# Kernel tuning notes

Hardware: AMD Instinct MI355X
Metric: run time of the kernel (lower is better)

The kernel has to match this reference:

```python
import jax, jax.numpy as jnp
import numpy as np

B = 262144
H = 64  # hidden size
T = 64  # timesteps


def _linear_params(key, out_dim, in_dim):
    k1, k2 = jax.random.split(key)
    bound = 1.0 / np.sqrt(in_dim)
    w = jax.random.uniform(k1, (out_dim, in_dim), jnp.float32, -bound, bound)
    b = jax.random.uniform(k2, (out_dim,), jnp.float32, -bound, bound)
    return w, b


def setup_inputs() -> dict:
    key = jax.random.key(0)
    ks = jax.random.split(key, 16)
    x = jax.random.normal(ks[0], (B, H), jnp.float32)
    W1, B1 = _linear_params(ks[1], H, 64)
    W2, B2 = _linear_params(ks[2], 64, 64)
    W3, B3 = _linear_params(ks[3], 64, 64)
    W4, B4 = _linear_params(ks[4], 64, 64)
    # mogrifier list (mogrify_steps=5): even idx Linear(hidden->input=1), odd idx Linear(input=1->hidden)
    M0w, M0b = _linear_params(ks[5], 1, H)
    M1w, M1b = _linear_params(ks[6], H, 1)
    M2w, M2b = _linear_params(ks[7], 1, H)
    M3w, M3b = _linear_params(ks[8], H, 1)
    M4w, M4b = _linear_params(ks[9], 1, H)
    # LSTMCell(input_size=1, hidden_size=64): gates order i,f,g,o
    Wih, Bih = _linear_params(ks[10], 4 * H, 1)
    Whh, Bhh = _linear_params(ks[11], 4 * H, H)
    Wp, Bp = _linear_params(ks[12], 5, H)
    return dict(x=x, W1=W1, B1=B1, W2=W2, B2=B2, W3=W3, B3=B3, W4=W4, B4=B4,
                M0w=M0w, M0b=M0b, M1w=M1w, M1b=M1b, M2w=M2w, M2b=M2b,
                M3w=M3w, M3b=M3b, M4w=M4w, M4b=M4b,
                Wih=Wih, Bih=Bih, Whh=Whh, Bhh=Bhh, Wp=Wp, Bp=Bp)


def _forward(x, W1, B1, W2, B2, W3, B3, W4, B4,
             M0w, M0b, M1w, M1b, M2w, M2b, M3w, M3b, M4w, M4b,
             Wih, Bih, Whh, Bhh, Wp, Bp):
    sig = jax.nn.sigmoid
    # MLP stem
    x = jax.nn.relu(x @ W1.T + B1)
    x = jax.nn.relu(x @ W2.T + B2)
    x = jax.nn.relu(x @ W3.T + B3)
    x = jax.nn.relu(x @ W4.T + B4)
    xs = x.T[:, :, None]  # (T, B, 1) time-major sequence of scalar inputs

    def step(carry, x_t):
        h, c = carry
        xt = x_t  # (B, 1)
        # mogrify: 5 alternating gating steps
        xt = 2.0 * sig(h @ M0w.T + M0b) * xt
        h = 2.0 * sig(xt @ M1w.T + M1b) * h
        xt = 2.0 * sig(h @ M2w.T + M2b) * xt
        h = 2.0 * sig(xt @ M3w.T + M3b) * h
        xt = 2.0 * sig(h @ M4w.T + M4b) * xt
        # LSTM cell
        gates = xt @ Wih.T + Bih + h @ Whh.T + Bhh  # (B, 4H)
        i, f, g, o = jnp.split(gates, 4, axis=-1)
        c = sig(f) * c + sig(i) * jnp.tanh(g)
        h = sig(o) * jnp.tanh(c)
        return (h, c), None

    h0 = jnp.zeros((x.shape[0], H), x.dtype)
    c0 = jnp.zeros((x.shape[0], H), x.dtype)
    (hT, _), _ = jax.lax.scan(step, (h0, c0), xs)
    return hT @ Wp.T + Bp  # (B, 5)


def reference(x, W1, B1, W2, B2, W3, B3, W4, B4,
              M0w, M0b, M1w, M1b, M2w, M2b, M3w, M3b, M4w, M4b,
              Wih, Bih, Whh, Bhh, Wp, Bp):
    return _forward(x, W1, B1, W2, B2, W3, B3, W4, B4,
                    M0w, M0b, M1w, M1b, M2w, M2b, M3w, M3b, M4w, M4b,
                    Wih, Bih, Whh, Bhh, Wp, Bp)
```

## Files before the change

### kernel.cpp

```cpp
#include <hip/hip_runtime.h>

#define HID 64
#define TSTEPS 64
#define NTHREADS 256
#define ROWS_PB 64

typedef __attribute__((ext_vector_type(8))) short bf16x8;
typedef __attribute__((ext_vector_type(4))) float f32x4;

__device__ __forceinline__ float fast_exp2(float x) { return __builtin_amdgcn_exp2f(x); }
__device__ __forceinline__ float fast_rcp(float x)  { return __builtin_amdgcn_rcpf(x); }
#define LOG2E 1.44269504088896341f
#define TWO_L 2.88539008177792682f

__device__ __forceinline__ unsigned short f2bf(float f) {
    unsigned u = __float_as_uint(f);
    u = u + 0x7fffu + ((u >> 16) & 1u);
    return (unsigned short)(u >> 16);
}
__device__ __forceinline__ float bfh(unsigned short h) { return __uint_as_float(((unsigned)h) << 16); }
__device__ __forceinline__ unsigned cvt_pk_bf16(float a, float b) {
    unsigned r;
    asm("v_cvt_pk_bf16_f32 %0, %1, %2" : "=v"(r) : "v"(a), "v"(b));
    return r;
}

__device__ __forceinline__ int permk(int p) {
    return (p & 0x23) | ((p & 0x04) << 2) | ((p & 0x18) >> 1);
}

#define OFF_WA    0
#define OFF_EXT   32768
#define OFF_ZERO  36864
#define OFF_MOGB  36880
#define OFF_XSEQ  40960
#define SMEM_TOTAL 49152

#define M0W 0
#define M2W 64
#define M4W 128
#define M1W 192
#define M1B 256
#define M3W 320
#define M3B 384
#define WPo 448
#define BPo 768

__global__ __launch_bounds__(NTHREADS, 2) void moglstm_mfma9(
    const float* __restrict__ x,
    const float* __restrict__ W1, const float* __restrict__ B1,
    const float* __restrict__ W2, const float* __restrict__ B2,
    const float* __restrict__ W3, const float* __restrict__ B3,
    const float* __restrict__ W4, const float* __restrict__ B4,
    const float* __restrict__ M0w, const float* __restrict__ M0b,
    const float* __restrict__ M1w, const float* __restrict__ M1b,
    const float* __restrict__ M2w, const float* __restrict__ M2b,
    const float* __restrict__ M3w, const float* __restrict__ M3b,
    const float* __restrict__ M4w, const float* __restrict__ M4b,
    const float* __restrict__ Wih, const float* __restrict__ Bih,
    const float* __restrict__ Whh, const float* __restrict__ Bhh,
    const float* __restrict__ Wp,  const float* __restrict__ Bp,
    float* __restrict__ out)
{
    __shared__ __align__(16) char smem[SMEM_TOTAL];
    bf16x8*   WA     = (bf16x8*)(smem + OFF_WA);
    float*    mogf   = (float*)(smem + OFF_MOGB);
    _Float16* sXseqH = (_Float16*)(smem + OFF_XSEQ);
    float*    ping   = (float*)(smem);
    float*    pong   = (float*)(smem + 17408);

    const int tid = threadIdx.x;
    const long rowbase = (long)blockIdx.x * ROWS_PB;

    for (int i = tid; i < ROWS_PB * 16; i += NTHREADS) {
        int r = i >> 4, c4 = i & 15;
        *(float4*)&ping[r * 68 + c4 * 4] = ((const float4*)x)[(rowbase + r) * 16 + c4];
    }
    __syncthreads();
    {
        const int sr = tid & 63;
        const int sq = tid >> 6;
        const float* Ws[4] = {W1, W2, W3, W4};
        const float* Bs[4] = {B1, B2, B3, B4};
        float rin[HID];
        #pragma unroll
        for (int L = 0; L < 4; ++L) {
            const float* SRC = (L & 1) ? pong : ping;
            float* DST       = (L & 1) ? ping : pong;
            #pragma unroll
            for (int k4 = 0; k4 < 16; ++k4) {
                float4 v = *(const float4*)&SRC[sr * 68 + k4 * 4];
                rin[4*k4+0] = v.x; rin[4*k4+1] = v.y; rin[4*k4+2] = v.z; rin[4*k4+3] = v.w;
            }
            __syncthreads();
            const float* W = Ws[L];
            const float* Bb = Bs[L];
            #pragma unroll
            for (int jj4 = 0; jj4 < 4; ++jj4) {
                float o[4];
                #pragma unroll
                for (int e = 0; e < 4; ++e) {
                    int j = sq * 16 + jj4 * 4 + e;
                    float a = Bb[j];
                    const float4* wr = (const float4*)(W + j * 64);
                    #pragma unroll
                    for (int k4 = 0; k4 < 16; ++k4) {
                        float4 w = wr[k4];
                        a += w.x*rin[4*k4] + w.y*rin[4*k4+1] + w.z*rin[4*k4+2] + w.w*rin[4*k4+3];
                    }
                    o[e] = fmaxf(a, 0.0f);
                }
                *(float4*)&DST[sr * 68 + sq * 16 + jj4 * 4] = make_float4(o[0], o[1], o[2], o[3]);
            }
            __syncthreads();
        }
    }

    for (int i = tid; i < TSTEPS * ROWS_PB; i += NTHREADS) {
        int t = i >> 6, r = i & 63;
        sXseqH[i] = (_Float16)ping[r * 68 + t];
    }
    __syncthreads();

    for (int i = tid; i < 2048; i += NTHREADS) {
        int ln = i & 63, kc = (i >> 6) & 1, tt = i >> 7;
        int gi = tt >> 2, u = tt & 3;
        int r = ln & 15, g = ln >> 4;
        float scl = (gi == 2) ? TWO_L : -LOG2E;
        const float* src = Whh + (gi * 64 + u * 16 + r) * 64;
        union { bf16x8 v; unsigned short s[8]; } f;
        #pragma unroll
        for (int j = 0; j < 8; ++j)
            f.s[j] = f2bf(scl * src[kc * 32 + 16 * (j >> 2) + 4 * g + (j & 3)]);
        WA[(tt * 2 + kc) * 64 + ln] = f.v;
    }
    {
        int tt = tid >> 4, r = tid & 15;
        int gi = tt >> 2;
        float scl = (gi == 2) ? TWO_L : -LOG2E;
        int G = gi * 64 + (tt & 3) * 16 + r;
        float wih = scl * Wih[G];
        float gb  = scl * (Bih[G] + Bhh[G]);
        unsigned short wh = f2bf(wih);
        unsigned short wl = f2bf(wih - bfh(wh));
        unsigned short gh = f2bf(gb);
        unsigned short gl = f2bf(gb - bfh(gh));
        union { bf16x8 v; unsigned u[4]; } f;
        f.u[0] = (unsigned)wh | ((unsigned)wh << 16);
        f.u[1] = (unsigned)wl | ((unsigned)gh << 16);
        f.u[2] = (unsigned)gl;
        f.u[3] = 0u;
        *(bf16x8*)(smem + OFF_EXT + tt * 256 + r * 16) = f.v;
    }
    if (tid < 4) ((float*)(smem + OFF_ZERO))[tid] = 0.0f;
    if (tid < 64) {
        int s = permk(tid);
        mogf[M0W + tid] = -LOG2E * M0w[s];
        mogf[M2W + tid] = -LOG2E * M2w[s];
        mogf[M4W + tid] = -LOG2E * M4w[s];
        mogf[M1W + tid] = -LOG2E * M1w[s];
        mogf[M1B + tid] = -LOG2E * M1b[s];
        mogf[M3W + tid] = -LOG2E * M3w[s];
        mogf[M3B + tid] = -LOG2E * M3b[s];
    }
    for (int i = tid; i < 320; i += NTHREADS)
        mogf[WPo + i] = Wp[(i & ~63) + permk(i & 63)];
    if (tid < 5) mogf[BPo + tid] = Bp[tid];
    __syncthreads();

    const int lane = tid & 63;
    const int wv   = tid >> 6;
    const int g_   = lane >> 4;
    const int n    = lane & 15;
    const int myrow = wv * 16 + n;

    const char* extb    = smem + ((g_ == 0) ? (OFF_EXT + n * 16) : OFF_ZERO);
    const int   extstep = (g_ == 0) ? 256 : 0;
    const float m0b_s = -LOG2E * M0b[0];
    const float m2b_s = -LOG2E * M2b[0];
    const float m4b_s = -LOG2E * M4b[0];

    float hB[16];
    f32x4 cst[4];
    #pragma unroll
    for (int i = 0; i < 16; ++i) hB[i] = 0.0f;
    #pragma unroll
    for (int u = 0; u < 4; ++u) cst[u] = (f32x4){0.0f, 0.0f, 0.0f, 0.0f};

#define MOG_DOT(MOFF, BIAS)                                                   \
    {                                                                         \
        float4 w0 = *(const float4*)&mogf[(MOFF) + g_ * 8];                   \
        float4 w1 = *(const float4*)&mogf[(MOFF) + g_ * 8 + 4];               \
        float4 w2 = *(const float4*)&mogf[(MOFF) + 32 + g_ * 8];              \
        float4 w3 = *(const float4*)&mogf[(MOFF) + 32 + g_ * 8 + 4];          \
        float p = w0.x*hB[0] + w0.y*hB[1] + w0.z*hB[2] + w0.w*hB[3]           \
                + w1.x*hB[4] + w1.y*hB[5] + w1.z*hB[6] + w1.w*hB[7]           \
                + w2.x*hB[8] + w2.y*hB[9] + w2.z*hB[10] + w2.w*hB[11]         \
                + w3.x*hB[12] + w3.y*hB[13] + w3.z*hB[14] + w3.w*hB[15];      \
        p += __shfl_xor(p, 16);                                               \
        p += __shfl_xor(p, 32);                                               \
        float t_ = fast_exp2(p + (BIAS));                                     \
        xt *= fast_rcp(0.5f + 0.5f * t_);                                     \
    }

#define MOG_SCALE(WOFF, BOFF)                                                 \
    {                                                                         \
        _Pragma("unroll")                                                     \
        for (int kc = 0; kc < 2; ++kc) {                                      \
            _Pragma("unroll")                                                 \
            for (int q = 0; q < 2; ++q) {                                     \
                float4 w4 = *(const float4*)&mogf[(WOFF) + kc*32 + g_*8 + q*4]; \
                float4 b4 = *(const float4*)&mogf[(BOFF) + kc*32 + g_*8 + q*4]; \
                int bse = kc * 8 + q * 4;                                     \
                hB[bse+0] *= fast_rcp(0.5f + 0.5f * fast_exp2(xt * w4.x + b4.x)); \
                hB[bse+1] *= fast_rcp(0.5f + 0.5f * fast_exp2(xt * w4.y + b4.y)); \
                hB[bse+2] *= fast_rcp(0.5f + 0.5f * fast_exp2(xt * w4.z + b4.z)); \
                hB[bse+3] *= fast_rcp(0.5f + 0.5f * fast_exp2(xt * w4.w + b4.w)); \
            }                                                                 \
        }                                                                     \
    }

    #pragma unroll 1
    for (int t = 0; t < TSTEPS; ++t) {
        float xt = (float)sXseqH[t * 64 + myrow];

        MOG_DOT(M0W, m0b_s)
        MOG_SCALE(M1W, M1B)
        MOG_DOT(M2W, m2b_s)
        MOG_SCALE(M3W, M3B)
        MOG_DOT(M4W, m4b_s)

        union uf8 { bf16x8 v; unsigned u[4]; };
        uf8 bhi0, bhi1, blo0, blo1, bext;
        #pragma unroll
        for (int kc = 0; kc < 2; ++kc) {
            #pragma unroll
            for (int jp = 0; jp < 4; ++jp) {
                float a = hB[kc * 8 + 2 * jp], b = hB[kc * 8 + 2 * jp + 1];
                unsigned hi = cvt_pk_bf16(a, b);
                float ah = __uint_as_float(hi << 16);
                float bh = __uint_as_float(hi & 0xffff0000u);
                unsigned lo = cvt_pk_bf16(a - ah, b - bh);
                if (kc == 0) { bhi0.u[jp] = hi; blo0.u[jp] = lo; }
                else         { bhi1.u[jp] = hi; blo1.u[jp] = lo; }
            }
        }
        {
            unsigned xh = cvt_pk_bf16(xt, xt) & 0xffffu;
            float xl = xt - bfh((unsigned short)xh);
            unsigned xlp = cvt_pk_bf16(xl, xl) & 0xffffu;
            bext.u[0] = xh | (xlp << 16);
            bext.u[1] = xh | (0x3F80u << 16);
            bext.u[2] = 0x3F80u;
            bext.u[3] = 0u;
        }

        auto gate_tile = [&](int tt) -> f32x4 {
            bf16x8 whi0 = WA[(tt * 2 + 0) * 64 + lane];
            bf16x8 whi1 = WA[(tt * 2 + 1) * 64 + lane];
            bf16x8 wext = *(const bf16x8*)(extb + tt * extstep);
            f32x4 d = {0.0f, 0.0f, 0.0f, 0.0f};
            d = __builtin_amdgcn_mfma_f32_16x16x32_bf16(wext, bext.v, d, 0, 0, 0);
            d = __builtin_amdgcn_mfma_f32_16x16x32_bf16(whi0, bhi0.v, d, 0, 0, 0);
            d = __builtin_amdgcn_mfma_f32_16x16x32_bf16(whi1, bhi1.v, d, 0, 0, 0);
            d = __builtin_amdgcn_mfma_f32_16x16x32_bf16(whi0, blo0.v, d, 0, 0, 0);
            d = __builtin_amdgcn_mfma_f32_16x16x32_bf16(whi1, blo1.v, d, 0, 0, 0);
            return d;
        };

        #pragma unroll
        for (int u = 0; u < 4; ++u) {
            f32x4 ai = gate_tile(u);
            f32x4 af = gate_tile(4 + u);
            f32x4 ag = gate_tile(8 + u);
            f32x4 ao = gate_tile(12 + u);
            #pragma unroll
            for (int e = 0; e < 4; ++e) {
                float A  = fast_exp2(ai[e]);
                float Bg = fminf(fast_exp2(ag[e]), 3.0e8f);
                float r  = fast_rcp((1.0f + A) * (1.0f + Bg));
                float p1 = (Bg - 1.0f) * r;
                float sf = fast_rcp(1.0f + fast_exp2(af[e]));
                float cc = sf * cst[u][e] + p1;
                cst[u][e] = cc;
                float Ao = fast_exp2(ao[e]);
                float Bc = fminf(fast_exp2(TWO_L * cc), 3.0e8f);
                float rc = fast_rcp((1.0f + Ao) * (1.0f + Bc));
                hB[u * 4 + e] = (Bc - 1.0f) * rc;
            }
        }
    }

    #pragma unroll
    for (int p = 0; p < 5; ++p) {
        float ap = 0.0f;
        #pragma unroll
        for (int kc = 0; kc < 2; ++kc) {
            #pragma unroll
            for (int q = 0; q < 2; ++q) {
                float4 w = *(const float4*)&mogf[WPo + p * 64 + kc * 32 + g_ * 8 + q * 4];
                ap += w.x * hB[kc * 8 + q * 4 + 0] + w.y * hB[kc * 8 + q * 4 + 1]
                    + w.z * hB[kc * 8 + q * 4 + 2] + w.w * hB[kc * 8 + q * 4 + 3];
            }
        }
        ap += __shfl_xor(ap, 16);
        ap += __shfl_xor(ap, 32);
        if (g_ == 0)
            out[(rowbase + myrow) * 5 + p] = ap + mogf[BPo + p];
    }
}

extern "C" void kernel_launch(void* const* d_in, const int* in_sizes, int n_in,
                              void* d_out, int out_size, void* d_ws, size_t ws_size,
                              hipStream_t stream) {
    const float* x   = (const float*)d_in[0];
    const float* W1  = (const float*)d_in[1];
    const float* B1  = (const float*)d_in[2];
    const float* W2  = (const float*)d_in[3];
    const float* B2  = (const float*)d_in[4];
    const float* W3  = (const float*)d_in[5];
    const float* B3  = (const float*)d_in[6];
    const float* W4  = (const float*)d_in[7];
    const float* B4  = (const float*)d_in[8];
    const float* M0w = (const float*)d_in[9];
    const float* M0b = (const float*)d_in[10];
    const float* M1w = (const float*)d_in[11];
    const float* M1b = (const float*)d_in[12];
    const float* M2w = (const float*)d_in[13];
    const float* M2b = (const float*)d_in[14];
    const float* M3w = (const float*)d_in[15];
    const float* M3b = (const float*)d_in[16];
    const float* M4w = (const float*)d_in[17];
    const float* M4b = (const float*)d_in[18];
    const float* Wih = (const float*)d_in[19];
    const float* Bih = (const float*)d_in[20];
    const float* Whh = (const float*)d_in[21];
    const float* Bhh = (const float*)d_in[22];
    const float* Wp  = (const float*)d_in[23];
    const float* Bp  = (const float*)d_in[24];

    int B = in_sizes[0] / HID;
    int nblocks = B / ROWS_PB;

    hipLaunchKernelGGL(moglstm_mfma9, dim3(nblocks), dim3(NTHREADS), 0, stream,
                       x, W1, B1, W2, B2, W3, B3, W4, B4,
                       M0w, M0b, M1w, M1b, M2w, M2b, M3w, M3b, M4w, M4b,
                       Wih, Bih, Whh, Bhh, Wp, Bp, (float*)d_out);
}
```

Measured before the change: 2.189 ms.

## Process two independent row tiles per wave to interleave recurrent MFMA chains

```diff
diff --git a/kernel.cpp b/kernel.cpp
--- a/kernel.cpp
+++ b/kernel.cpp
@@ -3,7 +3,7 @@
 #define HID 64
 #define TSTEPS 64
 #define NTHREADS 256
-#define ROWS_PB 64
+#define ROWS_PB 128
 
 typedef __attribute__((ext_vector_type(8))) short bf16x8;
 typedef __attribute__((ext_vector_type(4))) float f32x4;
@@ -34,7 +34,7 @@
 #define OFF_ZERO  36864
 #define OFF_MOGB  36880
 #define OFF_XSEQ  40960
-#define SMEM_TOTAL 49152
+#define SMEM_TOTAL 57344
 
 #define M0W 0
 #define M2W 64
@@ -46,7 +46,7 @@
 #define WPo 448
 #define BPo 768
 
-__global__ __launch_bounds__(NTHREADS, 2) void moglstm_mfma9(
+__global__ __launch_bounds__(NTHREADS, 2) void moglstm_dual(
     const float* __restrict__ x,
     const float* __restrict__ W1, const float* __restrict__ B1,
     const float* __restrict__ W2, const float* __restrict__ B2,
@@ -66,41 +66,38 @@
     bf16x8*   WA     = (bf16x8*)(smem + OFF_WA);
     float*    mogf   = (float*)(smem + OFF_MOGB);
     _Float16* sXseqH = (_Float16*)(smem + OFF_XSEQ);
-    float*    ping   = (float*)(smem);
-    float*    pong   = (float*)(smem + 17408);
+    float*    buf    = (float*)(smem);
 
     const int tid = threadIdx.x;
     const long rowbase = (long)blockIdx.x * ROWS_PB;
 
     for (int i = tid; i < ROWS_PB * 16; i += NTHREADS) {
         int r = i >> 4, c4 = i & 15;
-        *(float4*)&ping[r * 68 + c4 * 4] = ((const float4*)x)[(rowbase + r) * 16 + c4];
+        *(float4*)&buf[r * 68 + c4 * 4] = ((const float4*)x)[(rowbase + r) * 16 + c4];
     }
     __syncthreads();
     {
-        const int sr = tid & 63;
-        const int sq = tid >> 6;
+        const int sr = tid & 127;
+        const int sq = tid >> 7;
         const float* Ws[4] = {W1, W2, W3, W4};
         const float* Bs[4] = {B1, B2, B3, B4};
         float rin[HID];
         #pragma unroll
         for (int L = 0; L < 4; ++L) {
-            const float* SRC = (L & 1) ? pong : ping;
-            float* DST       = (L & 1) ? ping : pong;
             #pragma unroll
             for (int k4 = 0; k4 < 16; ++k4) {
-                float4 v = *(const float4*)&SRC[sr * 68 + k4 * 4];
+                float4 v = *(const float4*)&buf[sr * 68 + k4 * 4];
                 rin[4*k4+0] = v.x; rin[4*k4+1] = v.y; rin[4*k4+2] = v.z; rin[4*k4+3] = v.w;
             }
             __syncthreads();
             const float* W = Ws[L];
             const float* Bb = Bs[L];
             #pragma unroll
-            for (int jj4 = 0; jj4 < 4; ++jj4) {
+            for (int jj4 = 0; jj4 < 8; ++jj4) {
                 float o[4];
                 #pragma unroll
                 for (int e = 0; e < 4; ++e) {
-                    int j = sq * 16 + jj4 * 4 + e;
+                    int j = sq * 32 + jj4 * 4 + e;
                     float a = Bb[j];
                     const float4* wr = (const float4*)(W + j * 64);
                     #pragma unroll
@@ -110,15 +107,15 @@
                     }
                     o[e] = fmaxf(a, 0.0f);
                 }
-                *(float4*)&DST[sr * 68 + sq * 16 + jj4 * 4] = make_float4(o[0], o[1], o[2], o[3]);
+                *(float4*)&buf[sr * 68 + sq * 32 + jj4 * 4] = make_float4(o[0], o[1], o[2], o[3]);
             }
             __syncthreads();
         }
     }
 
     for (int i = tid; i < TSTEPS * ROWS_PB; i += NTHREADS) {
-        int t = i >> 6, r = i & 63;
-        sXseqH[i] = (_Float16)ping[r * 68 + t];
+        int t = i >> 7, r = i & 127;
+        sXseqH[i] = (_Float16)buf[r * 68 + t];
     }
     __syncthreads();
 
@@ -172,7 +169,8 @@
     const int wv   = tid >> 6;
     const int g_   = lane >> 4;
     const int n    = lane & 15;
-    const int myrow = wv * 16 + n;
+    const int r1 = wv * 32 + n;
+    const int r2 = wv * 32 + 16 + n;
 
     const char* extb    = smem + ((g_ == 0) ? (OFF_EXT + n * 16) : OFF_ZERO);
     const int   extstep = (g_ == 0) ? 256 : 0;
@@ -180,30 +178,40 @@
     const float m2b_s = -LOG2E * M2b[0];
     const float m4b_s = -LOG2E * M4b[0];
 
-    float hB[16];
-    f32x4 cst[4];
+    float hB1[16], hB2[16];
+    f32x4 cst1[4], cst2[4];
     #pragma unroll
-    for (int i = 0; i < 16; ++i) hB[i] = 0.0f;
+    for (int i = 0; i < 16; ++i) { hB1[i] = 0.0f; hB2[i] = 0.0f; }
     #pragma unroll
-    for (int u = 0; u < 4; ++u) cst[u] = (f32x4){0.0f, 0.0f, 0.0f, 0.0f};
-
-#define MOG_DOT(MOFF, BIAS)                                                   \
+    for (int u = 0; u < 4; ++u) {
+        cst1[u] = (f32x4){0.0f, 0.0f, 0.0f, 0.0f};
+        cst2[u] = (f32x4){0.0f, 0.0f, 0.0f, 0.0f};
+    }
+
+#define MOG_DOT2(MOFF, BIAS)                                                  \
     {                                                                         \
         float4 w0 = *(const float4*)&mogf[(MOFF) + g_ * 8];                   \
         float4 w1 = *(const float4*)&mogf[(MOFF) + g_ * 8 + 4];               \
         float4 w2 = *(const float4*)&mogf[(MOFF) + 32 + g_ * 8];              \
         float4 w3 = *(const float4*)&mogf[(MOFF) + 32 + g_ * 8 + 4];          \
-        float p = w0.x*hB[0] + w0.y*hB[1] + w0.z*hB[2] + w0.w*hB[3]           \
-                + w1.x*hB[4] + w1.y*hB[5] + w1.z*hB[6] + w1.w*hB[7]           \
-                + w2.x*hB[8] + w2.y*hB[9] + w2.z*hB[10] + w2.w*hB[11]         \
-                + w3.x*hB[12] + w3.y*hB[13] + w3.z*hB[14] + w3.w*hB[15];      \
-        p += __shfl_xor(p, 16);                                               \
-        p += __shfl_xor(p, 32);                                               \
-        float t_ = fast_exp2(p + (BIAS));                                     \
-        xt *= fast_rcp(0.5f + 0.5f * t_);                                     \
-    }
-
-#define MOG_SCALE(WOFF, BOFF)                                                 \
+        float pa1 = w0.x*hB1[0] + w0.y*hB1[1] + w0.z*hB1[2] + w0.w*hB1[3]     \
+                  + w1.x*hB1[4] + w1.y*hB1[5] + w1.z*hB1[6] + w1.w*hB1[7];    \
+        float pb1 = w2.x*hB1[8] + w2.y*hB1[9] + w2.z*hB1[10] + w2.w*hB1[11]   \
+                  + w3.x*hB1[12] + w3.y*hB1[13] + w3.z*hB1[14] + w3.w*hB1[15];\
+        float pa2 = w0.x*hB2[0] + w0.y*hB2[1] + w0.z*hB2[2] + w0.w*hB2[3]     \
+                  + w1.x*hB2[4] + w1.y*hB2[5] + w1.z*hB2[6] + w1.w*hB2[7];    \
+        float pb2 = w2.x*hB2[8] + w2.y*hB2[9] + w2.z*hB2[10] + w2.w*hB2[11]   \
+                  + w3.x*hB2[12] + w3.y*hB2[13] + w3.z*hB2[14] + w3.w*hB2[15];\
+        float p1 = pa1 + pb1, p2 = pa2 + pb2;                                 \
+        p1 += __shfl_xor(p1, 16);                                             \
+        p2 += __shfl_xor(p2, 16);                                             \
+        p1 += __shfl_xor(p1, 32);                                             \
+        p2 += __shfl_xor(p2, 32);                                             \
+        xt1 *= fast_rcp(0.5f + 0.5f * fast_exp2(p1 + (BIAS)));                \
+        xt2 *= fast_rcp(0.5f + 0.5f * fast_exp2(p2 + (BIAS)));                \
+    }
+
+#define MOG_SCALE2(WOFF, BOFF)                                                \
     {                                                                         \
         _Pragma("unroll")                                                     \
         for (int kc = 0; kc < 2; ++kc) {                                      \
@@ -212,101 +220,128 @@
                 float4 w4 = *(const float4*)&mogf[(WOFF) + kc*32 + g_*8 + q*4]; \
                 float4 b4 = *(const float4*)&mogf[(BOFF) + kc*32 + g_*8 + q*4]; \
                 int bse = kc * 8 + q * 4;                                     \
-                hB[bse+0] *= fast_rcp(0.5f + 0.5f * fast_exp2(xt * w4.x + b4.x)); \
-                hB[bse+1] *= fast_rcp(0.5f + 0.5f * fast_exp2(xt * w4.y + b4.y)); \
-                hB[bse+2] *= fast_rcp(0.5f + 0.5f * fast_exp2(xt * w4.z + b4.z)); \
-                hB[bse+3] *= fast_rcp(0.5f + 0.5f * fast_exp2(xt * w4.w + b4.w)); \
+                hB1[bse+0] *= fast_rcp(0.5f + 0.5f * fast_exp2(xt1 * w4.x + b4.x)); \
+                hB2[bse+0] *= fast_rcp(0.5f + 0.5f * fast_exp2(xt2 * w4.x + b4.x)); \
+                hB1[bse+1] *= fast_rcp(0.5f + 0.5f * fast_exp2(xt1 * w4.y + b4.y)); \
+                hB2[bse+1] *= fast_rcp(0.5f + 0.5f * fast_exp2(xt2 * w4.y + b4.y)); \
+                hB1[bse+2] *= fast_rcp(0.5f + 0.5f * fast_exp2(xt1 * w4.z + b4.z)); \
+                hB2[bse+2] *= fast_rcp(0.5f + 0.5f * fast_exp2(xt2 * w4.z + b4.z)); \
+                hB1[bse+3] *= fast_rcp(0.5f + 0.5f * fast_exp2(xt1 * w4.w + b4.w)); \
+                hB2[bse+3] *= fast_rcp(0.5f + 0.5f * fast_exp2(xt2 * w4.w + b4.w)); \
             }                                                                 \
         }                                                                     \
     }
 
+#define MKFRAGS(HB, XT, BHI0, BHI1, BLO0, BLO1, BEXT)                         \
+    {                                                                         \
+        _Pragma("unroll")                                                     \
+        for (int kc = 0; kc < 2; ++kc) {                                      \
+            _Pragma("unroll")                                                 \
+            for (int jp = 0; jp < 4; ++jp) {                                  \
+                float a = HB[kc * 8 + 2 * jp], b = HB[kc * 8 + 2 * jp + 1];   \
+                unsigned hi = cvt_pk_bf16(a, b);                              \
+                float ah = __uint_as_float(hi << 16);                         \
+                float bh = __uint_as_float(hi & 0xffff0000u);                 \
+                unsigned lo = cvt_pk_bf16(a - ah, b - bh);                    \
+                if (kc == 0) { BHI0.u[jp] = hi; BLO0.u[jp] = lo; }            \
+                else         { BHI1.u[jp] = hi; BLO1.u[jp] = lo; }            \
+            }                                                                 \
+        }                                                                     \
+        unsigned xh = cvt_pk_bf16(XT, XT) & 0xffffu;                          \
+        float xl = XT - bfh((unsigned short)xh);                              \
+        unsigned xlp = cvt_pk_bf16(xl, xl) & 0xffffu;                         \
+        BEXT.u[0] = xh | (xlp << 16);                                         \
+        BEXT.u[1] = xh | (0x3F80u << 16);                                     \
+        BEXT.u[2] = 0x3F80u;                                                  \
+        BEXT.u[3] = 0u;                                                       \
+    }
+
+#define ACT(AI, AF, AG, AO, CST, HB, U)                                       \
+    {                                                                         \
+        _Pragma("unroll")                                                     \
+        for (int e = 0; e < 4; ++e) {                                         \
+            float A  = fast_exp2(AI[e]);                                      \
+            float Bg = fminf(fast_exp2(AG[e]), 3.0e8f);                       \
+            float r  = fast_rcp((1.0f + A) * (1.0f + Bg));                    \
+            float p1v = (Bg - 1.0f) * r;                                      \
+            float sf = fast_rcp(1.0f + fast_exp2(AF[e]));                     \
+            float cc = sf * CST[U][e] + p1v;                                  \
+            CST[U][e] = cc;                                                   \
+            float Ao = fast_exp2(AO[e]);                                      \
+            float Bc = fminf(fast_exp2(TWO_L * cc), 3.0e8f);                  \
+            float rc = fast_rcp((1.0f + Ao) * (1.0f + Bc));                   \
+            HB[U * 4 + e] = (Bc - 1.0f) * rc;                                 \
+        }                                                                     \
+    }
+
     #pragma unroll 1
     for (int t = 0; t < TSTEPS; ++t) {
-        float xt = (float)sXseqH[t * 64 + myrow];
-
-        MOG_DOT(M0W, m0b_s)
-        MOG_SCALE(M1W, M1B)
-        MOG_DOT(M2W, m2b_s)
-        MOG_SCALE(M3W, M3B)
-        MOG_DOT(M4W, m4b_s)
+        float xt1 = (float)sXseqH[t * 128 + r1];
+        float xt2 = (float)sXseqH[t * 128 + r2];
+
+        MOG_DOT2(M0W, m0b_s)
+        MOG_SCALE2(M1W, M1B)
+        MOG_DOT2(M2W, m2b_s)
+        MOG_SCALE2(M3W, M3B)
+        MOG_DOT2(M4W, m4b_s)
 
         union uf8 { bf16x8 v; unsigned u[4]; };
-        uf8 bhi0, bhi1, blo0, blo1, bext;
-        #pragma unroll
-        for (int kc = 0; kc < 2; ++kc) {
-            #pragma unroll
-            for (int jp = 0; jp < 4; ++jp) {
-                float a = hB[kc * 8 + 2 * jp], b = hB[kc * 8 + 2 * jp + 1];
-                unsigned hi = cvt_pk_bf16(a, b);
-                float ah = __uint_as_float(hi << 16);
-                float bh = __uint_as_float(hi & 0xffff0000u);
-                unsigned lo = cvt_pk_bf16(a - ah, b - bh);
-                if (kc == 0) { bhi0.u[jp] = hi; blo0.u[jp] = lo; }
-                else         { bhi1.u[jp] = hi; blo1.u[jp] = lo; }
-            }
-        }
-        {
-            unsigned xh = cvt_pk_bf16(xt, xt) & 0xffffu;
-            float xl = xt - bfh((unsigned short)xh);
-            unsigned xlp = cvt_pk_bf16(xl, xl) & 0xffffu;
-            bext.u[0] = xh | (xlp << 16);
-            bext.u[1] = xh | (0x3F80u << 16);
-            bext.u[2] = 0x3F80u;
-            bext.u[3] = 0u;
-        }
-
-        auto gate_tile = [&](int tt) -> f32x4 {
-            bf16x8 whi0 = WA[(tt * 2 + 0) * 64 + lane];
-            bf16x8 whi1 = WA[(tt * 2 + 1) * 64 + lane];
-            bf16x8 wext = *(const bf16x8*)(extb + tt * extstep);
-            f32x4 d = {0.0f, 0.0f, 0.0f, 0.0f};
-            d = __builtin_amdgcn_mfma_f32_16x16x32_bf16(wext, bext.v, d, 0, 0, 0);
-            d = __builtin_amdgcn_mfma_f32_16x16x32_bf16(whi0, bhi0.v, d, 0, 0, 0);
-            d = __builtin_amdgcn_mfma_f32_16x16x32_bf16(whi1, bhi1.v, d, 0, 0, 0);
-            d = __builtin_amdgcn_mfma_f32_16x16x32_bf16(whi0, blo0.v, d, 0, 0, 0);
-            d = __builtin_amdgcn_mfma_f32_16x16x32_bf16(whi1, blo1.v, d, 0, 0, 0);
-            return d;
-        };
+        uf8 b1hi0, b1hi1, b1lo0, b1lo1, b1ext;
+        uf8 b2hi0, b2hi1, b2lo0, b2lo1, b2ext;
+        MKFRAGS(hB1, xt1, b1hi0, b1hi1, b1lo0, b1lo1, b1ext)
+        MKFRAGS(hB2, xt2, b2hi0, b2hi1, b2lo0, b2lo1, b2ext)
 
         #pragma unroll
         for (int u = 0; u < 4; ++u) {
-            f32x4 ai = gate_tile(u);
-            f32x4 af = gate_tile(4 + u);
-            f32x4 ag = gate_tile(8 + u);
-            f32x4 ao = gate_tile(12 + u);
+            f32x4 a1[4], a2[4];
             #pragma unroll
-            for (int e = 0; e < 4; ++e) {
-                float A  = fast_exp2(ai[e]);
-                float Bg = fminf(fast_exp2(ag[e]), 3.0e8f);
-                float r  = fast_rcp((1.0f + A) * (1.0f + Bg));
-                float p1 = (Bg - 1.0f) * r;
-                float sf = fast_rcp(1.0f + fast_exp2(af[e]));
-                float cc = sf * cst[u][e] + p1;
-                cst[u][e] = cc;
-                float Ao = fast_exp2(ao[e]);
-                float Bc = fminf(fast_exp2(TWO_L * cc), 3.0e8f);
-                float rc = fast_rcp((1.0f + Ao) * (1.0f + Bc));
-                hB[u * 4 + e] = (Bc - 1.0f) * rc;
+            for (int gi = 0; gi < 4; ++gi) {
+                const int tt = gi * 4 + u;
+                bf16x8 whi0 = WA[(tt * 2 + 0) * 64 + lane];
+                bf16x8 whi1 = WA[(tt * 2 + 1) * 64 + lane];
+                bf16x8 wext = *(const bf16x8*)(extb + tt * extstep);
+                f32x4 d1 = {0.0f, 0.0f, 0.0f, 0.0f};
+                f32x4 d2 = {0.0f, 0.0f, 0.0f, 0.0f};
+                d1 = __builtin_amdgcn_mfma_f32_16x16x32_bf16(wext, b1ext.v, d1, 0, 0, 0);
+                d2 = __builtin_amdgcn_mfma_f32_16x16x32_bf16(wext, b2ext.v, d2, 0, 0, 0);
+                d1 = __builtin_amdgcn_mfma_f32_16x16x32_bf16(whi0, b1hi0.v, d1, 0, 0, 0);
+                d2 = __builtin_amdgcn_mfma_f32_16x16x32_bf16(whi0, b2hi0.v, d2, 0, 0, 0);
+                d1 = __builtin_amdgcn_mfma_f32_16x16x32_bf16(whi1, b1hi1.v, d1, 0, 0, 0);
+                d2 = __builtin_amdgcn_mfma_f32_16x16x32_bf16(whi1, b2hi1.v, d2, 0, 0, 0);
+                d1 = __builtin_amdgcn_mfma_f32_16x16x32_bf16(whi0, b1lo0.v, d1, 0, 0, 0);
+                d2 = __builtin_amdgcn_mfma_f32_16x16x32_bf16(whi0, b2lo0.v, d2, 0, 0, 0);
+                d1 = __builtin_amdgcn_mfma_f32_16x16x32_bf16(whi1, b1lo1.v, d1, 0, 0, 0);
+                d2 = __builtin_amdgcn_mfma_f32_16x16x32_bf16(whi1, b2lo1.v, d2, 0, 0, 0);
+                a1[gi] = d1;
+                a2[gi] = d2;
             }
+            ACT(a1[0], a1[1], a1[2], a1[3], cst1, hB1, u)
+            ACT(a2[0], a2[1], a2[2], a2[3], cst2, hB2, u)
         }
     }
 
     #pragma unroll
     for (int p = 0; p < 5; ++p) {
-        float ap = 0.0f;
+        float ap1 = 0.0f, ap2 = 0.0f;
         #pragma unroll
         for (int kc = 0; kc < 2; ++kc) {
             #pragma unroll
             for (int q = 0; q < 2; ++q) {
                 float4 w = *(const float4*)&mogf[WPo + p * 64 + kc * 32 + g_ * 8 + q * 4];
-                ap += w.x * hB[kc * 8 + q * 4 + 0] + w.y * hB[kc * 8 + q * 4 + 1]
-                    + w.z * hB[kc * 8 + q * 4 + 2] + w.w * hB[kc * 8 + q * 4 + 3];
+                int bse = kc * 8 + q * 4;
+                ap1 += w.x * hB1[bse+0] + w.y * hB1[bse+1] + w.z * hB1[bse+2] + w.w * hB1[bse+3];
+                ap2 += w.x * hB2[bse+0] + w.y * hB2[bse+1] + w.z * hB2[bse+2] + w.w * hB2[bse+3];
             }
         }
-        ap += __shfl_xor(ap, 16);
-        ap += __shfl_xor(ap, 32);
-        if (g_ == 0)
-            out[(rowbase + myrow) * 5 + p] = ap + mogf[BPo + p];
+        ap1 += __shfl_xor(ap1, 16);
+        ap2 += __shfl_xor(ap2, 16);
+        ap1 += __shfl_xor(ap1, 32);
+        ap2 += __shfl_xor(ap2, 32);
+        if (g_ == 0) {
+            float bp = mogf[BPo + p];
+            out[(rowbase + r1) * 5 + p] = ap1 + bp;
+            out[(rowbase + r2) * 5 + p] = ap2 + bp;
+        }
     }
 }
 
@@ -342,7 +377,7 @@
     int B = in_sizes[0] / HID;
     int nblocks = B / ROWS_PB;
 
-    hipLaunchKernelGGL(moglstm_mfma9, dim3(nblocks), dim3(NTHREADS), 0, stream,
+    hipLaunchKernelGGL(moglstm_dual, dim3(nblocks), dim3(NTHREADS), 0, stream,
                        x, W1, B1, W2, B2, W3, B3, W4, B4,
                        M0w, M0b, M1w, M1b, M2w, M2b, M3w, M3b, M4w, M4b,
                        Wih, Bih, Whh, Bhh, Wp, Bp, (float*)d_out);
```

Result: slower. 2.551 ms (+16.5%).
